# Performance work log

Measured on AMD Instinct MI355X. Metric: run time of the kernel, lower is better.

Reference implementation:

```python
import jax, jax.numpy as jnp
import numpy as np

N_W, N_E, N_NUC, D_H = 8192, 32, 8, 32


def _init_linear(k, fan_in, fan_out):
    k1, k2 = jax.random.split(k)
    bound = 1.0 / np.sqrt(fan_in)
    W = jax.random.uniform(k1, (fan_in, fan_out), jnp.float32, -bound, bound)
    b = jax.random.uniform(k2, (fan_out,), jnp.float32, -bound, bound)
    return W, b


def setup_inputs() -> dict:
    key = jax.random.key(0)
    ks = jax.random.split(key, 12)
    W1_en, b1_en = _init_linear(ks[4], N_NUC, D_H)
    W2_en, b2_en = _init_linear(ks[5], D_H, D_H)
    W3_en, b3_en = _init_linear(ks[6], D_H, 1)
    W1_ee, b1_ee = _init_linear(ks[7], 1, D_H)
    W2_ee, b2_ee = _init_linear(ks[8], D_H, D_H)
    W3_ee, b3_ee = _init_linear(ks[9], D_H, 1)
    return {
        "r_electrons": jax.random.normal(ks[0], (N_W, N_E, 3), jnp.float32),
        "r_nuclei": jax.random.normal(ks[1], (N_NUC, 3), jnp.float32),
        "charges": jax.random.uniform(ks[2], (N_NUC,), jnp.float32),
        "spin_mask_parallel": jax.random.randint(ks[3], (N_E, N_E), 0, 2).astype(bool),
        "b_en": jnp.ones((N_NUC,), jnp.float32),
        "b_ee": jnp.array(1.0, jnp.float32),
        "W1_en": W1_en, "b1_en": b1_en, "W2_en": W2_en, "b2_en": b2_en,
        "W3_en": W3_en, "b3_en": b3_en,
        "W1_ee": W1_ee, "b1_ee": b1_ee, "W2_ee": W2_ee, "b2_ee": b2_ee,
        "W3_ee": W3_ee, "b3_ee": b3_ee,
        "scale_en": jnp.array(0.1, jnp.float32),
        "scale_ee": jnp.array(0.1, jnp.float32),
    }


def _mlp(x, W1, b1, W2, b2, W3, b3):
    h = jax.nn.silu(x @ W1 + b1)
    h = jax.nn.silu(h @ W2 + b2)
    return h @ W3 + b3


def reference(r_electrons, r_nuclei, charges, spin_mask_parallel,
              b_en, b_ee,
              W1_en, b1_en, W2_en, b2_en, W3_en, b3_en,
              W1_ee, b1_ee, W2_ee, b2_ee, W3_ee, b3_ee,
              scale_en, scale_ee):
    # --- electron-nucleus term ---
    d_en = r_electrons[:, :, None, :] - r_nuclei[None, None, :, :]  # [W,E,Nuc,3]
    r_en = jnp.linalg.norm(d_en, axis=-1)                            # [W,E,Nuc]
    b_en_s = jax.nn.softplus(b_en)
    J_en = jnp.sum(-charges * r_en / (1.0 + b_en_s * r_en), axis=(1, 2))  # [W]
    # r^2-killed neural correction (Linear over nuclei dim)
    J_en_nn = scale_en * jnp.sum(
        _mlp(r_en ** 2, W1_en, b1_en, W2_en, b2_en, W3_en, b3_en)[..., 0], axis=1)
    # --- electron-electron term (upper-triangular pairs only) ---
    iu, ju = np.triu_indices(N_E, k=1)  # static pair index lists, P = E*(E-1)/2
    diff = r_electrons[:, iu, :] - r_electrons[:, ju, :]  # [W,P,3]
    r_ee = jnp.linalg.norm(diff, axis=-1)                  # [W,P]
    a = jnp.where(spin_mask_parallel[iu, ju], 0.25, 0.5)   # [P]
    b_ee_s = jax.nn.softplus(b_ee)
    J_ee = jnp.sum(a * r_ee / (1.0 + b_ee_s * r_ee), axis=1)  # [W]
    J_ee_nn = scale_ee * jnp.sum(
        _mlp(r_ee[..., None], W1_ee, b1_ee, W2_ee, b2_ee, W3_ee, b3_ee)[..., 0], axis=1)
    return J_en + J_en_nn + J_ee + J_ee_nn
```

## Files before the change

### kernel.cpp

```cpp
#include <hip/hip_runtime.h>

#define N_W   8192
#define N_E   32
#define N_NUC 8
#define D_H   32
#define NTAB  2048
#define TAB_INVH 128.0f
#define TAB_H    (1.0f/128.0f)
#define WPB   8

#define AUX_OFF  8192
#define MSK_OFF  8208
#define W3S_OFF  8224
#define B_OFF    8256

typedef __attribute__((ext_vector_type(8)))  short bf16x8_t;
typedef __attribute__((ext_vector_type(16))) float f32x16_t;

union FragAB { bf16x8_t s; unsigned u[4]; };

__device__ __forceinline__ float fast_rcp(float x) { return __builtin_amdgcn_rcpf(x); }
__device__ __forceinline__ float silu_f(float v)   { return v * fast_rcp(1.0f + __expf(-v)); }
__device__ __forceinline__ unsigned pk_bf16(float lo, float hi) {
    unsigned r;
    asm("v_cvt_pk_bf16_f32 %0, %1, %2" : "=v"(r) : "v"(lo), "v"(hi));
    return r;
}

__global__ void build_tables(const float* __restrict__ W1ee, const float* __restrict__ b1ee,
                             const float* __restrict__ W2ee, const float* __restrict__ b2ee,
                             const float* __restrict__ W3ee, const float* __restrict__ b3ee,
                             const float* __restrict__ scale_ee,
                             const float* __restrict__ b_en, const float* __restrict__ b_ee,
                             const int* __restrict__ mask,
                             const float* __restrict__ W2en, const float* __restrict__ W3en,
                             const float* __restrict__ b3en, const float* __restrict__ scale_en,
                             float* __restrict__ ws)
{
    const int tid = threadIdx.x;
    if (blockIdx.x == 0) {
        float* aux = ws + AUX_OFF;
        if (tid < N_NUC) aux[tid] = __logf(1.0f + __expf(b_en[tid]));
        if (tid == 8)    aux[8]   = __logf(1.0f + __expf(b_ee[0]));
        if (tid == 9)    aux[9]   = 32.0f * scale_en[0] * b3en[0];
        if (tid < D_H)   ws[W3S_OFF + tid] = W3en[tid] * scale_en[0];
        if (tid < 16) {
            unsigned m = 0;
            int d = tid + 1;
            for (int e = 0; e < N_E; ++e) {
                int jn = (e + d) & 31;
                int a = e < jn ? e : jn, b = e < jn ? jn : e;
                if (mask[a * N_E + b]) m |= (1u << e);
            }
            ((unsigned*)(ws + MSK_OFF))[tid] = m;
        }
        unsigned* wsB = (unsigned*)(ws + B_OFF);
#pragma unroll
        for (int q = 0; q < 2; ++q) {
            int idx = tid + q * 256;
            int lane = idx >> 3, slot = idx & 7;
            int m2 = slot >> 2, r = slot & 3;
            int k = m2 * 16 + ((lane >> 5) << 3) + (r << 1);
            int j = lane & 31;
            wsB[lane * 8 + slot] = pk_bf16(W2en[k * D_H + j], W2en[(k + 1) * D_H + j]);
        }
    }
    const int j     = tid & 31;
    const int entry = blockIdx.x * 8 + (tid >> 5);
    const float bs  = __logf(1.0f + __expf(b_ee[0]));
    float mlp[2];
#pragma unroll
    for (int t = 0; t < 2; ++t) {
        float r = ((float)entry + (float)t) * TAB_H;
        float g = b2ee[j];
#pragma unroll
        for (int k = 0; k < D_H; ++k) g += silu_f(r * W1ee[k] + b1ee[k]) * W2ee[k * D_H + j];
        float o = silu_f(g) * W3ee[j];
#pragma unroll
        for (int m = 16; m; m >>= 1) o += __shfl_xor(o, m, 32);
        mlp[t] = scale_ee[0] * (o + b3ee[0]);
    }
    if (j == 0) {
        float r0 = (float)entry * TAB_H, r1 = r0 + TAB_H;
        float c0 = r0 * fast_rcp(1.0f + bs * r0);
        float c1 = r1 * fast_rcp(1.0f + bs * r1);
        *(float4*)(ws + 4 * entry) = make_float4(c0, c1 - c0, mlp[0], mlp[1] - mlp[0]);
    }
}

__launch_bounds__(256, 4)
__global__ void jastrow_kernel(const float* __restrict__ re, const float* __restrict__ rnuc,
                               const float* __restrict__ charges,
                               const float* __restrict__ W1, const float* __restrict__ b1,
                               const float* __restrict__ b2,
                               const float* __restrict__ ws,
                               float* __restrict__ out)
{
    const int tid  = threadIdx.x;
    const int e    = tid & 31;
    const int half = (tid >> 5) & 1;
    const int v    = tid >> 5;
    const int w    = blockIdx.x * WPB + v;
    const float* aux = ws + AUX_OFF;

    const float* cb = re + ((size_t)w * N_E + e) * 3;
    float ex = cb[0], ey = cb[1], ez = cb[2];

    float acc = 0.0f;

    float x[N_NUC];
#pragma unroll
    for (int n = 0; n < N_NUC; ++n) {
        float dx = ex - rnuc[n * 3 + 0];
        float dy = ey - rnuc[n * 3 + 1];
        float dz = ez - rnuc[n * 3 + 2];
        float r2 = dx * dx + dy * dy + dz * dz;
        x[n] = r2;
        float r = sqrtf(r2);
        acc -= charges[n] * r * fast_rcp(1.0f + aux[n] * r);
    }

    float2 hh[D_H / 2];
#pragma unroll
    for (int j = 0; j < D_H / 2; ++j) hh[j] = ((const float2*)b1)[j];
#pragma unroll
    for (int k = 0; k < N_NUC; ++k) {
        float xk = x[k];
        const float2* row = (const float2*)(W1 + k * D_H);
#pragma unroll
        for (int j = 0; j < D_H / 2; ++j) {
            float2 wv = row[j];
            hh[j].x = fmaf(xk, wv.x, hh[j].x);
            hh[j].y = fmaf(xk, wv.y, hh[j].y);
        }
    }
    unsigned hpk[16];
#pragma unroll
    for (int i = 0; i < 16; ++i) hpk[i] = pk_bf16(silu_f(hh[i].x), silu_f(hh[i].y));
    unsigned sx[16];
#pragma unroll
    for (int i = 0; i < 16; ++i) sx[i] = (unsigned)__shfl_xor((int)hpk[i], 32, 64);

    FragAB B1, B2;
    {
        const unsigned* wsB = (const unsigned*)(ws + B_OFF) + (size_t)(tid & 63) * 8;
        uint4 q0 = *(const uint4*)wsB;
        uint4 q1 = *(const uint4*)(wsB + 4);
        B1.u[0] = q0.x; B1.u[1] = q0.y; B1.u[2] = q0.z; B1.u[3] = q0.w;
        B2.u[0] = q1.x; B2.u[1] = q1.y; B2.u[2] = q1.z; B2.u[3] = q1.w;
    }
    const bool lo = (tid & 32) == 0;
    FragAB A1a, A2a, A1b, A2b;
#pragma unroll
    for (int r = 0; r < 4; ++r) {
        A1a.u[r] = lo ? hpk[r]      : sx[4 + r];
        A2a.u[r] = lo ? hpk[8 + r]  : sx[12 + r];
        A1b.u[r] = lo ? sx[r]       : hpk[4 + r];
        A2b.u[r] = lo ? sx[8 + r]   : hpk[12 + r];
    }
    float vb2 = b2[e];
    f32x16_t accA, accB;
#pragma unroll
    for (int r = 0; r < 16; ++r) { accA[r] = vb2; accB[r] = vb2; }
    accA = __builtin_amdgcn_mfma_f32_32x32x16_bf16(A1a.s, B1.s, accA, 0, 0, 0);
    accA = __builtin_amdgcn_mfma_f32_32x32x16_bf16(A2a.s, B2.s, accA, 0, 0, 0);
    accB = __builtin_amdgcn_mfma_f32_32x32x16_bf16(A1b.s, B1.s, accB, 0, 0, 0);
    accB = __builtin_amdgcn_mfma_f32_32x32x16_bf16(A2b.s, B2.s, accB, 0, 0, 0);

    float w3s = ws[W3S_OFF + e];
    float sA = 0.0f, sB = 0.0f;
#pragma unroll
    for (int r = 0; r < 16; ++r) { sA += silu_f(accA[r]); sB += silu_f(accB[r]); }
    float mlpA = sA * w3s, mlpB = sB * w3s;

    unsigned mks[16];
    {
        const unsigned* mp = (const unsigned*)(ws + MSK_OFF);
#pragma unroll
        for (int i = 0; i < 16; ++i) mks[i] = mp[i];
    }
#pragma unroll
    for (int d = 1; d <= 16; ++d) {
        int jn = (e + d) & 31;
        float cjx = __shfl(ex, jn, 32);
        float cjy = __shfl(ey, jn, 32);
        float cjz = __shfl(ez, jn, 32);
        float dx = ex - cjx, dy = ey - cjy, dz = ez - cjz;
        float r = sqrtf(dx * dx + dy * dy + dz * dz);
        float t = r * TAB_INVH;
        int i0 = (int)t;
        if (i0 > NTAB - 2) i0 = NTAB - 2;
        float f = t - (float)i0;
        float4 T = *(const float4*)(ws + 4 * i0);
        float a = ((mks[d - 1] >> e) & 1u) ? 0.25f : 0.5f;
        float pv = a * fmaf(f, T.y, T.x) + fmaf(f, T.w, T.z);
        acc += (d == 16) ? 0.5f * pv : pv;
    }

    float valA = mlpA + (half ? 0.0f : acc);
    float valB = mlpB + (half ? acc : 0.0f);
#pragma unroll
    for (int m = 32; m; m >>= 1) {
        valA += __shfl_xor(valA, m, 64);
        valB += __shfl_xor(valB, m, 64);
    }
    if ((tid & 63) == 0) {
        int wA = blockIdx.x * WPB + ((tid >> 6) << 1);
        out[wA]     = valA + aux[9];
        out[wA + 1] = valB + aux[9];
    }
}

extern "C" void kernel_launch(void* const* d_in, const int* in_sizes, int n_in,
                              void* d_out, int out_size, void* d_ws, size_t ws_size,
                              hipStream_t stream)
{
    const float* re       = (const float*)d_in[0];
    const float* rnuc     = (const float*)d_in[1];
    const float* charges  = (const float*)d_in[2];
    const int*   mask     = (const int*)d_in[3];
    const float* b_en     = (const float*)d_in[4];
    const float* b_ee     = (const float*)d_in[5];
    const float* W1_en    = (const float*)d_in[6];
    const float* b1_en    = (const float*)d_in[7];
    const float* W2_en    = (const float*)d_in[8];
    const float* b2_en    = (const float*)d_in[9];
    const float* W3_en    = (const float*)d_in[10];
    const float* b3_en    = (const float*)d_in[11];
    const float* W1_ee    = (const float*)d_in[12];
    const float* b1_ee    = (const float*)d_in[13];
    const float* W2_ee    = (const float*)d_in[14];
    const float* b2_ee    = (const float*)d_in[15];
    const float* W3_ee    = (const float*)d_in[16];
    const float* b3_ee    = (const float*)d_in[17];
    const float* scale_en = (const float*)d_in[18];
    const float* scale_ee = (const float*)d_in[19];

    float* out = (float*)d_out;
    float* ws  = (float*)d_ws;

    build_tables<<<NTAB / 8, 256, 0, stream>>>(W1_ee, b1_ee, W2_ee, b2_ee, W3_ee, b3_ee,
                                               scale_ee, b_en, b_ee, mask,
                                               W2_en, W3_en, b3_en, scale_en, ws);
    jastrow_kernel<<<N_W / WPB, 256, 0, stream>>>(re, rnuc, charges,
                                                  W1_en, b1_en, b2_en, ws, out);
}
```

Baseline: 22.71 us.

## Compute en-MLP first layer via MFMA and compact ee lookup table

The first layer of the electron-nucleus MLP now runs as an MFMA, with the bias folded in as an extra K column set to one. It replaces the per-thread scalar FMA loop over 8x32 weights, and the second layer switches to a transposed weights-as-A layout. The ee table shrinks from float4 (value and slope) to float2 nodes, with slopes computed at lookup time. Table build now uses 64 threads per entry split over K halves, across more blocks. This adds bf16 rounding of the r² inputs and extra shuffles and layout complexity.

```diff
diff --git a/kernel.cpp b/kernel.cpp
--- a/kernel.cpp
+++ b/kernel.cpp
@@ -9,10 +9,11 @@
 #define TAB_H    (1.0f/128.0f)
 #define WPB   8
 
-#define AUX_OFF  8192
-#define MSK_OFF  8208
-#define W3S_OFF  8224
-#define B_OFF    8256
+#define AUX_OFF 4096
+#define MSK_OFF 4112
+#define W3S_OFF 4128
+#define W1T_OFF 4160
+#define W2T_OFF 4416
 
 typedef __attribute__((ext_vector_type(8)))  short bf16x8_t;
 typedef __attribute__((ext_vector_type(16))) float f32x16_t;
@@ -33,6 +34,7 @@
                              const float* __restrict__ scale_ee,
                              const float* __restrict__ b_en, const float* __restrict__ b_ee,
                              const int* __restrict__ mask,
+                             const float* __restrict__ W1en, const float* __restrict__ b1en,
                              const float* __restrict__ W2en, const float* __restrict__ W3en,
                              const float* __restrict__ b3en, const float* __restrict__ scale_en,
                              float* __restrict__ ws)
@@ -43,64 +45,65 @@
         if (tid < N_NUC) aux[tid] = __logf(1.0f + __expf(b_en[tid]));
         if (tid == 8)    aux[8]   = __logf(1.0f + __expf(b_ee[0]));
         if (tid == 9)    aux[9]   = 32.0f * scale_en[0] * b3en[0];
-        if (tid < D_H)   ws[W3S_OFF + tid] = W3en[tid] * scale_en[0];
-        if (tid < 16) {
+        if (tid >= 32 && tid < 64) ws[W3S_OFF + tid - 32] = W3en[tid - 32] * scale_en[0];
+        if (tid >= 64 && tid < 80) {
+            int d = tid - 63;
             unsigned m = 0;
-            int d = tid + 1;
-            for (int e = 0; e < N_E; ++e) {
-                int jn = (e + d) & 31;
-                int a = e < jn ? e : jn, b = e < jn ? jn : e;
-                if (mask[a * N_E + b]) m |= (1u << e);
+            for (int e2 = 0; e2 < N_E; ++e2) {
+                int jn = (e2 + d) & 31;
+                int a = e2 < jn ? e2 : jn, b = e2 < jn ? jn : e2;
+                if (mask[a * N_E + b]) m |= (1u << e2);
             }
-            ((unsigned*)(ws + MSK_OFF))[tid] = m;
-        }
-        unsigned* wsB = (unsigned*)(ws + B_OFF);
+            ((unsigned*)(ws + MSK_OFF))[d - 1] = m;
+        }
+        {
+            int L = tid >> 2, r = tid & 3, j = L & 31;
+            unsigned u = 0;
+            if (L < 32)      u = pk_bf16(W1en[(2 * r) * D_H + j], W1en[(2 * r + 1) * D_H + j]);
+            else if (r == 0) u = pk_bf16(b1en[j], 0.0f);
+            ((unsigned*)(ws + W1T_OFF))[(L << 2) + r] = u;
+        }
 #pragma unroll
         for (int q = 0; q < 2; ++q) {
-            int idx = tid + q * 256;
-            int lane = idx >> 3, slot = idx & 7;
-            int m2 = slot >> 2, r = slot & 3;
-            int k = m2 * 16 + ((lane >> 5) << 3) + (r << 1);
-            int j = lane & 31;
-            wsB[lane * 8 + slot] = pk_bf16(W2en[k * D_H + j], W2en[(k + 1) * D_H + j]);
-        }
-    }
-    const int j     = tid & 31;
-    const int entry = blockIdx.x * 8 + (tid >> 5);
-    const float bs  = __logf(1.0f + __expf(b_ee[0]));
-    float mlp[2];
-#pragma unroll
-    for (int t = 0; t < 2; ++t) {
-        float r = ((float)entry + (float)t) * TAB_H;
-        float g = b2ee[j];
-#pragma unroll
-        for (int k = 0; k < D_H; ++k) g += silu_f(r * W1ee[k] + b1ee[k]) * W2ee[k * D_H + j];
-        float o = silu_f(g) * W3ee[j];
-#pragma unroll
-        for (int m = 16; m; m >>= 1) o += __shfl_xor(o, m, 32);
-        mlp[t] = scale_ee[0] * (o + b3ee[0]);
-    }
-    if (j == 0) {
-        float r0 = (float)entry * TAB_H, r1 = r0 + TAB_H;
-        float c0 = r0 * fast_rcp(1.0f + bs * r0);
-        float c1 = r1 * fast_rcp(1.0f + bs * r1);
-        *(float4*)(ws + 4 * entry) = make_float4(c0, c1 - c0, mlp[0], mlp[1] - mlp[0]);
+            int idx = tid + (q << 8);
+            int L = idx >> 3, s = idx & 7, j = L & 31;
+            int kb = ((L >> 5) << 3) + ((s & 3) << 1) + ((s >> 2) << 4);
+            ((unsigned*)(ws + W2T_OFF))[(L << 3) + s] =
+                pk_bf16(W2en[kb * D_H + j], W2en[(kb + 1) * D_H + j]);
+        }
+    }
+    const int entry = blockIdx.x * 4 + (tid >> 6);
+    const int j = tid & 31, kh = (tid >> 5) & 1;
+    const float r = (float)entry * TAB_H;
+    float g = kh ? 0.0f : b2ee[j];
+#pragma unroll
+    for (int kk = 0; kk < 16; ++kk) {
+        int k = kh * 16 + kk;
+        g += silu_f(r * W1ee[k] + b1ee[k]) * W2ee[k * D_H + j];
+    }
+    g += __shfl_xor(g, 32, 64);
+    float o = silu_f(g) * W3ee[j];
+#pragma unroll
+    for (int m = 16; m; m >>= 1) o += __shfl_xor(o, m, 32);
+    if ((tid & 63) == 0) {
+        float bs = __logf(1.0f + __expf(b_ee[0]));
+        float c = r * fast_rcp(1.0f + bs * r);
+        *(float2*)(ws + 2 * entry) = make_float2(c, scale_ee[0] * (o + b3ee[0]));
     }
 }
 
 __launch_bounds__(256, 4)
 __global__ void jastrow_kernel(const float* __restrict__ re, const float* __restrict__ rnuc,
                                const float* __restrict__ charges,
-                               const float* __restrict__ W1, const float* __restrict__ b1,
                                const float* __restrict__ b2,
                                const float* __restrict__ ws,
                                float* __restrict__ out)
 {
     const int tid  = threadIdx.x;
     const int e    = tid & 31;
-    const int half = (tid >> 5) & 1;
-    const int v    = tid >> 5;
-    const int w    = blockIdx.x * WPB + v;
+    const int lane = tid & 63;
+    const bool lo  = (tid & 32) == 0;
+    const int w    = blockIdx.x * WPB + (tid >> 5);
     const float* aux = ws + AUX_OFF;
 
     const float* cb = re + ((size_t)w * N_E + e) * 3;
@@ -120,58 +123,79 @@
         acc -= charges[n] * r * fast_rcp(1.0f + aux[n] * r);
     }
 
-    float2 hh[D_H / 2];
-#pragma unroll
-    for (int j = 0; j < D_H / 2; ++j) hh[j] = ((const float2*)b1)[j];
-#pragma unroll
-    for (int k = 0; k < N_NUC; ++k) {
-        float xk = x[k];
-        const float2* row = (const float2*)(W1 + k * D_H);
-#pragma unroll
-        for (int j = 0; j < D_H / 2; ++j) {
-            float2 wv = row[j];
-            hh[j].x = fmaf(xk, wv.x, hh[j].x);
-            hh[j].y = fmaf(xk, wv.y, hh[j].y);
-        }
-    }
-    unsigned hpk[16];
-#pragma unroll
-    for (int i = 0; i < 16; ++i) hpk[i] = pk_bf16(silu_f(hh[i].x), silu_f(hh[i].y));
-    unsigned sx[16];
-#pragma unroll
-    for (int i = 0; i < 16; ++i) sx[i] = (unsigned)__shfl_xor((int)hpk[i], 32, 64);
-
-    FragAB B1, B2;
-    {
-        const unsigned* wsB = (const unsigned*)(ws + B_OFF) + (size_t)(tid & 63) * 8;
-        uint4 q0 = *(const uint4*)wsB;
-        uint4 q1 = *(const uint4*)(wsB + 4);
-        B1.u[0] = q0.x; B1.u[1] = q0.y; B1.u[2] = q0.z; B1.u[3] = q0.w;
-        B2.u[0] = q1.x; B2.u[1] = q1.y; B2.u[2] = q1.z; B2.u[3] = q1.w;
-    }
-    const bool lo = (tid & 32) == 0;
-    FragAB A1a, A2a, A1b, A2b;
+    unsigned xpk[4], sxp[4];
+#pragma unroll
+    for (int r = 0; r < 4; ++r) xpk[r] = pk_bf16(x[2 * r], x[2 * r + 1]);
+#pragma unroll
+    for (int r = 0; r < 4; ++r) sxp[r] = (unsigned)__shfl_xor((int)xpk[r], 32, 64);
+
+    FragAB B1A, B1B;
 #pragma unroll
     for (int r = 0; r < 4; ++r) {
-        A1a.u[r] = lo ? hpk[r]      : sx[4 + r];
-        A2a.u[r] = lo ? hpk[8 + r]  : sx[12 + r];
-        A1b.u[r] = lo ? sx[r]       : hpk[4 + r];
-        A2b.u[r] = lo ? sx[8 + r]   : hpk[12 + r];
-    }
-    float vb2 = b2[e];
-    f32x16_t accA, accB;
-#pragma unroll
-    for (int r = 0; r < 16; ++r) { accA[r] = vb2; accB[r] = vb2; }
-    accA = __builtin_amdgcn_mfma_f32_32x32x16_bf16(A1a.s, B1.s, accA, 0, 0, 0);
-    accA = __builtin_amdgcn_mfma_f32_32x32x16_bf16(A2a.s, B2.s, accA, 0, 0, 0);
-    accB = __builtin_amdgcn_mfma_f32_32x32x16_bf16(A1b.s, B1.s, accB, 0, 0, 0);
-    accB = __builtin_amdgcn_mfma_f32_32x32x16_bf16(A2b.s, B2.s, accB, 0, 0, 0);
-
-    float w3s = ws[W3S_OFF + e];
-    float sA = 0.0f, sB = 0.0f;
-#pragma unroll
-    for (int r = 0; r < 16; ++r) { sA += silu_f(accA[r]); sB += silu_f(accB[r]); }
-    float mlpA = sA * w3s, mlpB = sB * w3s;
+        unsigned oneh = (r == 0) ? 0x00003F80u : 0u;
+        B1A.u[r] = lo ? xpk[r] : oneh;
+        B1B.u[r] = lo ? sxp[r] : oneh;
+    }
+    FragAB A1;
+    {
+        uint4 q = *((const uint4*)((const unsigned*)(ws + W1T_OFF) + (lane << 2)));
+        A1.u[0] = q.x; A1.u[1] = q.y; A1.u[2] = q.z; A1.u[3] = q.w;
+    }
+    f32x16_t z;
+#pragma unroll
+    for (int r = 0; r < 16; ++r) z[r] = 0.0f;
+    f32x16_t HA = __builtin_amdgcn_mfma_f32_32x32x16_bf16(A1.s, B1A.s, z, 0, 0, 0);
+    f32x16_t HB = __builtin_amdgcn_mfma_f32_32x32x16_bf16(A1.s, B1B.s, z, 0, 0, 0);
+
+    FragAB A2a, A2b;
+    {
+        const unsigned* p = (const unsigned*)(ws + W2T_OFF) + ((size_t)lane << 3);
+        uint4 q0 = *(const uint4*)p;
+        uint4 q1 = *(const uint4*)(p + 4);
+        A2a.u[0] = q0.x; A2a.u[1] = q0.y; A2a.u[2] = q0.z; A2a.u[3] = q0.w;
+        A2b.u[0] = q1.x; A2b.u[1] = q1.y; A2b.u[2] = q1.z; A2b.u[3] = q1.w;
+    }
+    float b2v[16], w3v[16];
+    {
+        const float* b2q = b2 + ((lane >> 5) << 2);
+        const float* w3q = ws + W3S_OFF + ((lane >> 5) << 2);
+#pragma unroll
+        for (int r = 0; r < 16; ++r) {
+            int ri = (r & 3) + ((r >> 2) << 3);
+            b2v[r] = b2q[ri];
+            w3v[r] = w3q[ri];
+        }
+    }
+
+    float sA, sB;
+#pragma unroll
+    for (int wk = 0; wk < 2; ++wk) {
+        const f32x16_t& H = wk ? HB : HA;
+        unsigned p[8], sx2[8];
+#pragma unroll
+        for (int i = 0; i < 8; ++i)
+            p[i] = pk_bf16(silu_f(H[2 * i]), silu_f(H[2 * i + 1]));
+#pragma unroll
+        for (int i = 0; i < 8; ++i) sx2[i] = (unsigned)__shfl_xor((int)p[i], 32, 64);
+        FragAB Ba, Bb;
+        Ba.u[0] = lo ? p[0]   : sx2[2];
+        Ba.u[1] = lo ? p[1]   : sx2[3];
+        Ba.u[2] = lo ? sx2[0] : p[2];
+        Ba.u[3] = lo ? sx2[1] : p[3];
+        Bb.u[0] = lo ? p[4]   : sx2[6];
+        Bb.u[1] = lo ? p[5]   : sx2[7];
+        Bb.u[2] = lo ? sx2[4] : p[6];
+        Bb.u[3] = lo ? sx2[5] : p[7];
+        f32x16_t g;
+#pragma unroll
+        for (int r = 0; r < 16; ++r) g[r] = b2v[r];
+        g = __builtin_amdgcn_mfma_f32_32x32x16_bf16(A2a.s, Ba.s, g, 0, 0, 0);
+        g = __builtin_amdgcn_mfma_f32_32x32x16_bf16(A2b.s, Bb.s, g, 0, 0, 0);
+        float s = 0.0f;
+#pragma unroll
+        for (int r = 0; r < 16; ++r) s += silu_f(g[r]) * w3v[r];
+        if (wk == 0) sA = s; else sB = s;
+    }
 
     unsigned mks[16];
     {
@@ -179,6 +203,7 @@
 #pragma unroll
         for (int i = 0; i < 16; ++i) mks[i] = mp[i];
     }
+    float bs = aux[8];
 #pragma unroll
     for (int d = 1; d <= 16; ++d) {
         int jn = (e + d) & 31;
@@ -191,14 +216,15 @@
         int i0 = (int)t;
         if (i0 > NTAB - 2) i0 = NTAB - 2;
         float f = t - (float)i0;
-        float4 T = *(const float4*)(ws + 4 * i0);
+        const float* np = ws + (i0 << 1);
+        float c0 = np[0], m0 = np[1], c1 = np[2], m1 = np[3];
         float a = ((mks[d - 1] >> e) & 1u) ? 0.25f : 0.5f;
-        float pv = a * fmaf(f, T.y, T.x) + fmaf(f, T.w, T.z);
+        float pv = a * fmaf(f, c1 - c0, c0) + fmaf(f, m1 - m0, m0);
         acc += (d == 16) ? 0.5f * pv : pv;
     }
 
-    float valA = mlpA + (half ? 0.0f : acc);
-    float valB = mlpB + (half ? acc : 0.0f);
+    float valA = sA + (lo ? acc : 0.0f);
+    float valB = sB + (lo ? 0.0f : acc);
 #pragma unroll
     for (int m = 32; m; m >>= 1) {
         valA += __shfl_xor(valA, m, 64);
@@ -239,9 +265,9 @@
     float* out = (float*)d_out;
     float* ws  = (float*)d_ws;
 
-    build_tables<<<NTAB / 8, 256, 0, stream>>>(W1_ee, b1_ee, W2_ee, b2_ee, W3_ee, b3_ee,
+    build_tables<<<NTAB / 4, 256, 0, stream>>>(W1_ee, b1_ee, W2_ee, b2_ee, W3_ee, b3_ee,
                                                scale_ee, b_en, b_ee, mask,
-                                               W2_en, W3_en, b3_en, scale_en, ws);
-    jastrow_kernel<<<N_W / WPB, 256, 0, stream>>>(re, rnuc, charges,
-                                                  W1_en, b1_en, b2_en, ws, out);
-}
+                                               W1_en, b1_en, W2_en, W3_en, b3_en, scale_en,
+                                               ws);
+    jastrow_kernel<<<N_W / WPB, 256, 0, stream>>>(re, rnuc, charges, b2_en, ws, out);
+}
```

Result: faster. 21.23 us (-6.5%).
